# Kernel tuning notes

Hardware: AMD Instinct MI355X
Metric: run time of the kernel (lower is better)

## Reference

```python
import jax, jax.numpy as jnp
import numpy as np

NUM_SAMPLE = 80  # hardcoded in the original forward
NUM_ACT = 6
NUM_OPP = 3


def setup_inputs() -> dict:
    key = jax.random.key(0)
    k0, k1, k2 = jax.random.split(key, 3)
    B, D = 4096, 512
    x = jax.random.normal(k0, (B, D), dtype=jnp.float32)
    # orthogonal init with gain 0.01 -> small weights; approximate scale
    W_opp = jax.random.normal(k1, (NUM_OPP, D, NUM_ACT), dtype=jnp.float32) * 0.01
    b_opp = jnp.zeros((NUM_OPP, NUM_ACT), dtype=jnp.float32)
    W = jax.random.normal(k2, (D + NUM_OPP * NUM_ACT, NUM_ACT), dtype=jnp.float32) * 0.01
    b = jnp.zeros((NUM_ACT,), dtype=jnp.float32)
    return {"x": x, "W_opp": W_opp, "b_opp": b_opp, "W": W, "b": b}


def reference(x, W_opp, b_opp, W, b):
    B, D = x.shape
    # --- opponent actors: small linear + softmax, vectorized over the 3 opponents ---
    logits = jnp.einsum('bd,kda->kba', x, W_opp) + b_opp[:, None, :]   # [3,B,6]
    dist = jax.nn.softmax(logits, axis=-1)                              # [3,B,6]
    logp = jax.nn.log_softmax(logits, axis=-1)
    # entropy.mean() per opponent, then sum/3 == mean over opponents
    entropy = (-(dist * logp).sum(-1)).mean(-1).mean()

    # --- vectorized categorical sampling: 80 samples per opponent per batch elem ---
    skey = jax.random.key(42)
    samples = jax.random.categorical(skey, logits[:, None], axis=-1,
                                     shape=(NUM_OPP, NUM_SAMPLE, B))   # [3,S,B] int

    # gather sampled-action probabilities
    probs = jnp.take_along_axis(dist[:, None], samples[..., None], axis=-1)[..., 0]  # [3,S,B]
    probs_bt = jnp.transpose(probs, (0, 2, 1))                          # [3,B,S]
    p1 = probs_bt[0] * probs_bt[1] * probs_bt[2]                        # [B,S]
    p2 = p1 / p1.sum(axis=1, keepdims=True)                             # normalized joint weights

    # actions3[b,s,k] = sampled action of opponent k, sample s, batch b
    acts = jnp.transpose(samples, (2, 1, 0))                            # [B,S,3]
    oh = jax.nn.one_hot(acts, NUM_ACT, dtype=x.dtype).reshape(B, NUM_SAMPLE, NUM_OPP * NUM_ACT)  # [B,S,18]

    xa = jnp.broadcast_to(x[:, None, :], (B, NUM_SAMPLE, D))            # replicate x per sample
    a = jnp.concatenate([xa, oh], axis=2)                               # [B,S,D+18]
    agent_probs = jax.nn.softmax(a @ W + b, axis=-1)                    # [B,S,6]

    actions_probs = jnp.einsum('bs,bsa->ba', p2, agent_probs)           # [B,6]
    return actions_probs, dist, entropy
```

## Files before the change

kernel.cpp:

```cpp
#include <hip/hip_runtime.h>
#include <stdint.h>

#define NUM_ACT 6
#define NUM_OPP 3
#define NUM_SAMPLE 80
#define BATCH 4096
#define DIM 512
#define ACC_STRIDE 98304
#define TROWS 32

__device__ __forceinline__ uint32_t rotl32(uint32_t x, int d) {
  return (x << d) | (x >> (32 - d));
}

__device__ __forceinline__ void tf_round4(uint32_t& x0, uint32_t& x1,
                                          int r0, int r1, int r2, int r3) {
  x0 += x1; x1 = rotl32(x1, r0); x1 ^= x0;
  x0 += x1; x1 = rotl32(x1, r1); x1 ^= x0;
  x0 += x1; x1 = rotl32(x1, r2); x1 ^= x0;
  x0 += x1; x1 = rotl32(x1, r3); x1 ^= x0;
}

__device__ __forceinline__ void threefry2x32(uint32_t k0, uint32_t k1,
                                             uint32_t& x0, uint32_t& x1) {
  const uint32_t ks2 = k0 ^ k1 ^ 0x1BD11BDAu;
  x0 += k0;  x1 += k1;
  tf_round4(x0, x1, 13, 15, 26, 6);  x0 += k1;  x1 += ks2 + 1u;
  tf_round4(x0, x1, 17, 29, 16, 24); x0 += ks2; x1 += k0  + 2u;
  tf_round4(x0, x1, 13, 15, 26, 6);  x0 += k0;  x1 += k1  + 3u;
  tf_round4(x0, x1, 17, 29, 16, 24); x0 += k1;  x1 += ks2 + 4u;
  tf_round4(x0, x1, 13, 15, 26, 6);  x0 += ks2; x1 += k0  + 5u;
}

__device__ __forceinline__ float jax_uniform(uint32_t flat_idx) {
  uint32_t x0 = 0u, x1 = flat_idx;
  threefry2x32(0u, 42u, x0, x1);
  uint32_t bits = x0 ^ x1;
  return __uint_as_float((bits >> 9) | 0x3f800000u) - 1.0f;
}

__device__ __forceinline__ void dot4(float& a, float4 u, float4 v) {
  a = fmaf(u.x, v.x, a); a = fmaf(u.y, v.y, a);
  a = fmaf(u.z, v.z, a); a = fmaf(u.w, v.w, a);
}

template<int NCH>
__global__ __launch_bounds__(128) void k1_gemm(
    const float* __restrict__ x, const float* __restrict__ Wopp,
    const float* __restrict__ W, float* __restrict__ part,
    float* __restrict__ ws_ent) {
  constexpr int WIDTH = 512 / NCH;
  constexpr int XSTR = WIDTH + 4;
  const int tile = blockIdx.x / NCH;
  const int ch = blockIdx.x % NCH;
  const int rowbase = tile * TROWS;
  const int dbase = ch * WIDTH;
  __shared__ float xs[TROWS * XSTR];
  __shared__ float wt[24 * XSTR];
  const int t = threadIdx.x;

  for (int f = t; f < TROWS * (WIDTH / 4); f += 128) {
    int row = f / (WIDTH / 4), c4 = (f % (WIDTH / 4)) << 2;
    float4 v = *(const float4*)(x + (size_t)(rowbase + row) * DIM + dbase + c4);
    *(float4*)(xs + row * XSTR + c4) = v;
  }
  for (int i = t; i < 24 * WIDTH; i += 128) {
    int c = i % 24, dd = i / 24;
    int d = dbase + dd;
    float v = (c < 18) ? Wopp[(c / 6) * (DIM * 6) + d * 6 + (c % 6)]
                       : W[d * 6 + (c - 18)];
    wt[c * XSTR + dd] = v;
  }
  __syncthreads();

  const int rowg = t >> 3, colg = t & 7;
  float acc[2][3] = {{0.f, 0.f, 0.f}, {0.f, 0.f, 0.f}};
  const float* xp = xs + (rowg * 2) * XSTR;
  const float* wp = wt + (colg * 3) * XSTR;
#pragma unroll 4
  for (int dd = 0; dd < WIDTH; dd += 4) {
    float4 x0 = *(const float4*)(xp + dd);
    float4 x1 = *(const float4*)(xp + XSTR + dd);
    float4 w0 = *(const float4*)(wp + dd);
    float4 w1 = *(const float4*)(wp + XSTR + dd);
    float4 w2 = *(const float4*)(wp + 2 * XSTR + dd);
    dot4(acc[0][0], x0, w0); dot4(acc[0][1], x0, w1); dot4(acc[0][2], x0, w2);
    dot4(acc[1][0], x1, w0); dot4(acc[1][1], x1, w1); dot4(acc[1][2], x1, w2);
  }
  const int r0 = rowbase + rowg * 2, c0 = colg * 3;
  float* p = part + (size_t)ch * ACC_STRIDE;
#pragma unroll
  for (int rr = 0; rr < 2; rr++)
#pragma unroll
    for (int cc = 0; cc < 3; cc++)
      p[(r0 + rr) * 24 + c0 + cc] = acc[rr][cc];
  if (blockIdx.x == 0 && t == 0) ws_ent[0] = 0.f;
}

template<int NCH>
__global__ __launch_bounds__(256) void k2_softmax(
    const float* __restrict__ part, const float* __restrict__ bopp,
    float* __restrict__ dout, float* __restrict__ ws_ent) {
  int row = blockIdx.x * 256 + threadIdx.x;
  int k = row >> 12, b = row & 4095;
  float l[NUM_ACT];
#pragma unroll
  for (int a = 0; a < NUM_ACT; a++) {
    float s = bopp[k * 6 + a];
#pragma unroll
    for (int ch = 0; ch < NCH; ch++)
      s += part[ch * ACC_STRIDE + b * 24 + k * 6 + a];
    l[a] = s;
  }
  float m = l[0];
#pragma unroll
  for (int a = 1; a < NUM_ACT; a++) m = fmaxf(m, l[a]);
  float e[NUM_ACT], Z = 0.f;
#pragma unroll
  for (int a = 0; a < NUM_ACT; a++) { e[a] = expf(l[a] - m); Z += e[a]; }
  float logZ = logf(Z);
  float H = 0.f;
#pragma unroll
  for (int a = 0; a < NUM_ACT; a++) {
    float pa = e[a] / Z;
    dout[BATCH * NUM_ACT + row * NUM_ACT + a] = pa;
    H -= pa * ((l[a] - m) - logZ);
  }
#pragma unroll
  for (int off = 32; off > 0; off >>= 1) H += __shfl_down(H, off);
  if ((threadIdx.x & 63) == 0) atomicAdd(ws_ent, H);
}

template<int NCH>
__global__ __launch_bounds__(256) void k3_agent(
    const float* __restrict__ part, const float* __restrict__ bopp,
    const float* __restrict__ W, const float* __restrict__ bias,
    const float* __restrict__ ws_ent, float* __restrict__ dout) {
  int b = blockIdx.x;
  int t = threadIdx.x;
  __shared__ float s_dist[NUM_OPP][NUM_ACT];
  __shared__ float s_xw[NUM_ACT];
  __shared__ float s_bias[NUM_ACT];
  __shared__ float s_W2[NUM_OPP * NUM_ACT][NUM_ACT];
  __shared__ int   s_act[NUM_OPP][NUM_SAMPLE];
  __shared__ float s_prob[NUM_OPP][NUM_SAMPLE];

  if (t < 18) {
    int k = t / 6, a = t - k * 6;
    s_dist[k][a] = dout[BATCH * NUM_ACT + (k * BATCH + b) * NUM_ACT + a];
  } else if (t >= 64 && t < 64 + NUM_ACT) {
    int a = t - 64;
    float s = bias[a];
#pragma unroll
    for (int ch = 0; ch < NCH; ch++)
      s += part[ch * ACC_STRIDE + b * 24 + 18 + a];
    s_xw[a] = s;
  } else if (t >= 128 && t < 128 + 108) {
    int i = t - 128;
    s_W2[i / 6][i % 6] = W[DIM * NUM_ACT + i];
  }
  __syncthreads();

  if (t < NUM_OPP * NUM_SAMPLE) {
    int k = t / NUM_SAMPLE, s = t - k * NUM_SAMPLE;
    float u = jax_uniform((uint32_t)(k * NUM_SAMPLE + s) * BATCH + (uint32_t)b);
    float c = s_dist[k][0], pr = s_dist[k][0];
    int sel = 0;
#pragma unroll
    for (int a = 1; a < NUM_ACT; a++) {
      bool take = (u >= c);
      sel += take ? 1 : 0;
      pr = take ? s_dist[k][a] : pr;
      c += s_dist[k][a];
    }
    s_act[k][s] = sel;
    s_prob[k][s] = pr;
  }
  __syncthreads();

  if (t < 64) {
    float p1a = s_prob[0][t] * s_prob[1][t] * s_prob[2][t];
    const bool hasb = t < (NUM_SAMPLE - 64);
    float p1b = 0.f;
    if (hasb) p1b = s_prob[0][t + 16] * s_prob[1][t + 16] * s_prob[2][t + 16];
    if (hasb) p1b = s_prob[0][t + 64] * s_prob[1][t + 64] * s_prob[2][t + 64];
    float tot = p1a + p1b;
#pragma unroll
    for (int m = 32; m > 0; m >>= 1) tot += __shfl_xor(tot, m);

    float o[NUM_ACT];
#pragma unroll
    for (int a = 0; a < NUM_ACT; a++) o[a] = 0.f;
    {
      int a0 = s_act[0][t], a1 = s_act[1][t], a2 = s_act[2][t];
      float la[NUM_ACT];
#pragma unroll
      for (int a = 0; a < NUM_ACT; a++)
        la[a] = s_xw[a] + s_W2[a0][a] + s_W2[6 + a1][a] + s_W2[12 + a2][a];
      float m = la[0];
#pragma unroll
      for (int a = 1; a < NUM_ACT; a++) m = fmaxf(m, la[a]);
      float e[NUM_ACT], Z = 0.f;
#pragma unroll
      for (int a = 0; a < NUM_ACT; a++) { e[a] = expf(la[a] - m); Z += e[a]; }
      float wz = (p1a / tot) / Z;
#pragma unroll
      for (int a = 0; a < NUM_ACT; a++) o[a] = wz * e[a];
    }
    if (hasb) {
      int j = t + 64;
      int a0 = s_act[0][j], a1 = s_act[1][j], a2 = s_act[2][j];
      float la[NUM_ACT];
#pragma unroll
      for (int a = 0; a < NUM_ACT; a++)
        la[a] = s_xw[a] + s_W2[a0][a] + s_W2[6 + a1][a] + s_W2[12 + a2][a];
      float m = la[0];
#pragma unroll
      for (int a = 1; a < NUM_ACT; a++) m = fmaxf(m, la[a]);
      float e[NUM_ACT], Z = 0.f;
#pragma unroll
      for (int a = 0; a < NUM_ACT; a++) { e[a] = expf(la[a] - m); Z += e[a]; }
      float wz = (p1b / tot) / Z;
#pragma unroll
      for (int a = 0; a < NUM_ACT; a++) o[a] += wz * e[a];
    }
#pragma unroll
    for (int m = 32; m > 0; m >>= 1)
#pragma unroll
      for (int a = 0; a < NUM_ACT; a++) o[a] += __shfl_xor(o[a], m);
    if (t == 0) {
#pragma unroll
      for (int a = 0; a < NUM_ACT; a++) dout[b * NUM_ACT + a] = o[a];
    }
  }
  if (b == 0 && t == 255) {
    dout[BATCH * NUM_ACT + NUM_OPP * BATCH * NUM_ACT] = ws_ent[0] * (1.0f / 12288.0f);
  }
}

extern "C" void kernel_launch(void* const* d_in, const int* in_sizes, int n_in,
                              void* d_out, int out_size, void* d_ws, size_t ws_size,
                              hipStream_t stream) {
  const float* x    = (const float*)d_in[0];
  const float* Wopp = (const float*)d_in[1];
  const float* bopp = (const float*)d_in[2];
  const float* W    = (const float*)d_in[3];
  const float* bias = (const float*)d_in[4];
  float* out = (float*)d_out;
  float* part = (float*)d_ws;

  size_t need8 = ((size_t)8 * ACC_STRIDE + 1) * sizeof(float);
  if (ws_size >= need8) {
    float* ws_ent = part + (size_t)8 * ACC_STRIDE;
    k1_gemm<8><<<(BATCH / TROWS) * 8, 128, 0, stream>>>(x, Wopp, W, part, ws_ent);
    k2_softmax<8><<<48, 256, 0, stream>>>(part, bopp, out, ws_ent);
    k3_agent<8><<<BATCH, 256, 0, stream>>>(part, bopp, W, bias, ws_ent, out);
  } else {
    float* ws_ent = part + (size_t)4 * ACC_STRIDE;
    k1_gemm<4><<<(BATCH / TROWS) * 4, 128, 0, stream>>>(x, Wopp, W, part, ws_ent);
    k2_softmax<4><<<48, 256, 0, stream>>>(part, bopp, out, ws_ent);
    k3_agent<4><<<BATCH, 256, 0, stream>>>(part, bopp, W, bias, ws_ent, out);
  }
}
```

Before: 90.33 us.

## Fuse GEMM, opponent softmax and agent sampling into one per-row kernel

Replaces the three-kernel pipeline (tiled GEMM writing partial sums to workspace, a softmax/entropy kernel, and a per-row agent kernel) with one kernel launched per batch row. Each block loads its x row into shared memory, computes the 24 dot products with 8-way split-K in shared memory, does the softmax, entropy atomic and sampling in place, and zeroes the entropy slot with a memset. This removes the workspace round trips and two launches. The cost is that the weight matrices are re-read from global memory by every block with strided scalar loads, and every block issues an atomic on the same address. It also drops a redundant dead load of p1b.

```diff
diff --git a/kernel.cpp b/kernel.cpp
--- a/kernel.cpp
+++ b/kernel.cpp
@@ -6,8 +6,7 @@
 #define NUM_SAMPLE 80
 #define BATCH 4096
 #define DIM 512
-#define ACC_STRIDE 98304
-#define TROWS 32
+#define ENT_IDX 98304
 
 __device__ __forceinline__ uint32_t rotl32(uint32_t x, int d) {
   return (x << d) | (x >> (32 - d));
@@ -39,130 +38,82 @@
   return __uint_as_float((bits >> 9) | 0x3f800000u) - 1.0f;
 }
 
-__device__ __forceinline__ void dot4(float& a, float4 u, float4 v) {
-  a = fmaf(u.x, v.x, a); a = fmaf(u.y, v.y, a);
-  a = fmaf(u.z, v.z, a); a = fmaf(u.w, v.w, a);
-}
-
-template<int NCH>
-__global__ __launch_bounds__(128) void k1_gemm(
+__global__ __launch_bounds__(256) void k_fused(
     const float* __restrict__ x, const float* __restrict__ Wopp,
-    const float* __restrict__ W, float* __restrict__ part,
-    float* __restrict__ ws_ent) {
-  constexpr int WIDTH = 512 / NCH;
-  constexpr int XSTR = WIDTH + 4;
-  const int tile = blockIdx.x / NCH;
-  const int ch = blockIdx.x % NCH;
-  const int rowbase = tile * TROWS;
-  const int dbase = ch * WIDTH;
-  __shared__ float xs[TROWS * XSTR];
-  __shared__ float wt[24 * XSTR];
+    const float* __restrict__ bopp, const float* __restrict__ W,
+    const float* __restrict__ bias, float* __restrict__ out) {
+  const int b = blockIdx.x;
   const int t = threadIdx.x;
 
-  for (int f = t; f < TROWS * (WIDTH / 4); f += 128) {
-    int row = f / (WIDTH / 4), c4 = (f % (WIDTH / 4)) << 2;
-    float4 v = *(const float4*)(x + (size_t)(rowbase + row) * DIM + dbase + c4);
-    *(float4*)(xs + row * XSTR + c4) = v;
-  }
-  for (int i = t; i < 24 * WIDTH; i += 128) {
-    int c = i % 24, dd = i / 24;
-    int d = dbase + dd;
-    float v = (c < 18) ? Wopp[(c / 6) * (DIM * 6) + d * 6 + (c % 6)]
-                       : W[d * 6 + (c - 18)];
-    wt[c * XSTR + dd] = v;
-  }
-  __syncthreads();
-
-  const int rowg = t >> 3, colg = t & 7;
-  float acc[2][3] = {{0.f, 0.f, 0.f}, {0.f, 0.f, 0.f}};
-  const float* xp = xs + (rowg * 2) * XSTR;
-  const float* wp = wt + (colg * 3) * XSTR;
-#pragma unroll 4
-  for (int dd = 0; dd < WIDTH; dd += 4) {
-    float4 x0 = *(const float4*)(xp + dd);
-    float4 x1 = *(const float4*)(xp + XSTR + dd);
-    float4 w0 = *(const float4*)(wp + dd);
-    float4 w1 = *(const float4*)(wp + XSTR + dd);
-    float4 w2 = *(const float4*)(wp + 2 * XSTR + dd);
-    dot4(acc[0][0], x0, w0); dot4(acc[0][1], x0, w1); dot4(acc[0][2], x0, w2);
-    dot4(acc[1][0], x1, w0); dot4(acc[1][1], x1, w1); dot4(acc[1][2], x1, w2);
-  }
-  const int r0 = rowbase + rowg * 2, c0 = colg * 3;
-  float* p = part + (size_t)ch * ACC_STRIDE;
-#pragma unroll
-  for (int rr = 0; rr < 2; rr++)
-#pragma unroll
-    for (int cc = 0; cc < 3; cc++)
-      p[(r0 + rr) * 24 + c0 + cc] = acc[rr][cc];
-  if (blockIdx.x == 0 && t == 0) ws_ent[0] = 0.f;
-}
-
-template<int NCH>
-__global__ __launch_bounds__(256) void k2_softmax(
-    const float* __restrict__ part, const float* __restrict__ bopp,
-    float* __restrict__ dout, float* __restrict__ ws_ent) {
-  int row = blockIdx.x * 256 + threadIdx.x;
-  int k = row >> 12, b = row & 4095;
-  float l[NUM_ACT];
-#pragma unroll
-  for (int a = 0; a < NUM_ACT; a++) {
-    float s = bopp[k * 6 + a];
-#pragma unroll
-    for (int ch = 0; ch < NCH; ch++)
-      s += part[ch * ACC_STRIDE + b * 24 + k * 6 + a];
-    l[a] = s;
-  }
-  float m = l[0];
-#pragma unroll
-  for (int a = 1; a < NUM_ACT; a++) m = fmaxf(m, l[a]);
-  float e[NUM_ACT], Z = 0.f;
-#pragma unroll
-  for (int a = 0; a < NUM_ACT; a++) { e[a] = expf(l[a] - m); Z += e[a]; }
-  float logZ = logf(Z);
-  float H = 0.f;
-#pragma unroll
-  for (int a = 0; a < NUM_ACT; a++) {
-    float pa = e[a] / Z;
-    dout[BATCH * NUM_ACT + row * NUM_ACT + a] = pa;
-    H -= pa * ((l[a] - m) - logZ);
-  }
-#pragma unroll
-  for (int off = 32; off > 0; off >>= 1) H += __shfl_down(H, off);
-  if ((threadIdx.x & 63) == 0) atomicAdd(ws_ent, H);
-}
-
-template<int NCH>
-__global__ __launch_bounds__(256) void k3_agent(
-    const float* __restrict__ part, const float* __restrict__ bopp,
-    const float* __restrict__ W, const float* __restrict__ bias,
-    const float* __restrict__ ws_ent, float* __restrict__ dout) {
-  int b = blockIdx.x;
-  int t = threadIdx.x;
+  __shared__ float xs[DIM];
+  __shared__ float s_part[8][24];
   __shared__ float s_dist[NUM_OPP][NUM_ACT];
   __shared__ float s_xw[NUM_ACT];
-  __shared__ float s_bias[NUM_ACT];
   __shared__ float s_W2[NUM_OPP * NUM_ACT][NUM_ACT];
   __shared__ int   s_act[NUM_OPP][NUM_SAMPLE];
   __shared__ float s_prob[NUM_OPP][NUM_SAMPLE];
 
-  if (t < 18) {
-    int k = t / 6, a = t - k * 6;
-    s_dist[k][a] = dout[BATCH * NUM_ACT + (k * BATCH + b) * NUM_ACT + a];
-  } else if (t >= 64 && t < 64 + NUM_ACT) {
-    int a = t - 64;
-    float s = bias[a];
-#pragma unroll
-    for (int ch = 0; ch < NCH; ch++)
-      s += part[ch * ACC_STRIDE + b * 24 + 18 + a];
-    s_xw[a] = s;
-  } else if (t >= 128 && t < 128 + 108) {
+  {
+    float2 v = *(const float2*)(x + (size_t)b * DIM + t * 2);
+    *(float2*)(xs + t * 2) = v;
+  }
+  if (t >= 128 && t < 128 + 108) {
     int i = t - 128;
     s_W2[i / 6][i % 6] = W[DIM * NUM_ACT + i];
   }
   __syncthreads();
 
+  if (t < 192) {
+    const int c = t % 24, g = t / 24;
+    const float* wp = (c < 18) ? (Wopp + (c / 6) * (DIM * NUM_ACT) + (c % 6))
+                               : (W + (c - 18));
+    wp += (size_t)(g * 64) * NUM_ACT;
+    const float* xp = xs + g * 64;
+    float acc = 0.f;
+#pragma unroll 8
+    for (int d = 0; d < 64; d++)
+      acc = fmaf(xp[d], wp[d * NUM_ACT], acc);
+    s_part[g][c] = acc;
+  }
+  __syncthreads();
+
+  if (t < NUM_OPP) {
+    const int k = t;
+    float l[NUM_ACT];
+#pragma unroll
+    for (int a = 0; a < NUM_ACT; a++) {
+      float s = bopp[k * NUM_ACT + a];
+#pragma unroll
+      for (int g = 0; g < 8; g++) s += s_part[g][k * NUM_ACT + a];
+      l[a] = s;
+    }
+    float m = l[0];
+#pragma unroll
+    for (int a = 1; a < NUM_ACT; a++) m = fmaxf(m, l[a]);
+    float e[NUM_ACT], Z = 0.f;
+#pragma unroll
+    for (int a = 0; a < NUM_ACT; a++) { e[a] = expf(l[a] - m); Z += e[a]; }
+    float logZ = logf(Z);
+    float H = 0.f;
+#pragma unroll
+    for (int a = 0; a < NUM_ACT; a++) {
+      float pa = e[a] / Z;
+      s_dist[k][a] = pa;
+      out[BATCH * NUM_ACT + ((size_t)k * BATCH + b) * NUM_ACT + a] = pa;
+      H -= pa * ((l[a] - m) - logZ);
+    }
+    atomicAdd(out + ENT_IDX, H * (1.0f / 12288.0f));
+  } else if (t >= 18 && t < 24) {
+    const int a = t - 18;
+    float s = bias[a];
+#pragma unroll
+    for (int g = 0; g < 8; g++) s += s_part[g][18 + a];
+    s_xw[a] = s;
+  }
+  __syncthreads();
+
   if (t < NUM_OPP * NUM_SAMPLE) {
-    int k = t / NUM_SAMPLE, s = t - k * NUM_SAMPLE;
+    const int k = t / NUM_SAMPLE, s = t - k * NUM_SAMPLE;
     float u = jax_uniform((uint32_t)(k * NUM_SAMPLE + s) * BATCH + (uint32_t)b);
     float c = s_dist[k][0], pr = s_dist[k][0];
     int sel = 0;
@@ -182,7 +133,6 @@
     float p1a = s_prob[0][t] * s_prob[1][t] * s_prob[2][t];
     const bool hasb = t < (NUM_SAMPLE - 64);
     float p1b = 0.f;
-    if (hasb) p1b = s_prob[0][t + 16] * s_prob[1][t + 16] * s_prob[2][t + 16];
     if (hasb) p1b = s_prob[0][t + 64] * s_prob[1][t + 64] * s_prob[2][t + 64];
     float tot = p1a + p1b;
 #pragma unroll
@@ -230,11 +180,8 @@
       for (int a = 0; a < NUM_ACT; a++) o[a] += __shfl_xor(o[a], m);
     if (t == 0) {
 #pragma unroll
-      for (int a = 0; a < NUM_ACT; a++) dout[b * NUM_ACT + a] = o[a];
-    }
-  }
-  if (b == 0 && t == 255) {
-    dout[BATCH * NUM_ACT + NUM_OPP * BATCH * NUM_ACT] = ws_ent[0] * (1.0f / 12288.0f);
+      for (int a = 0; a < NUM_ACT; a++) out[b * NUM_ACT + a] = o[a];
+    }
   }
 }
 
@@ -247,18 +194,7 @@
   const float* W    = (const float*)d_in[3];
   const float* bias = (const float*)d_in[4];
   float* out = (float*)d_out;
-  float* part = (float*)d_ws;
-
-  size_t need8 = ((size_t)8 * ACC_STRIDE + 1) * sizeof(float);
-  if (ws_size >= need8) {
-    float* ws_ent = part + (size_t)8 * ACC_STRIDE;
-    k1_gemm<8><<<(BATCH / TROWS) * 8, 128, 0, stream>>>(x, Wopp, W, part, ws_ent);
-    k2_softmax<8><<<48, 256, 0, stream>>>(part, bopp, out, ws_ent);
-    k3_agent<8><<<BATCH, 256, 0, stream>>>(part, bopp, W, bias, ws_ent, out);
-  } else {
-    float* ws_ent = part + (size_t)4 * ACC_STRIDE;
-    k1_gemm<4><<<(BATCH / TROWS) * 4, 128, 0, stream>>>(x, Wopp, W, part, ws_ent);
-    k2_softmax<4><<<48, 256, 0, stream>>>(part, bopp, out, ws_ent);
-    k3_agent<4><<<BATCH, 256, 0, stream>>>(part, bopp, W, bias, ws_ent, out);
-  }
-}
+
+  hipMemsetAsync(out + ENT_IDX, 0, sizeof(float), stream);
+  k_fused<<<BATCH, 256, 0, stream>>>(x, Wopp, bopp, W, bias, out);
+}
```

Measured after the change: 133.2 us. 1.47x slower.

## Fuse opponent softmax into per-wavefront agent kernel and reduce entropy deterministically

Applied to the files above, without the earlier changes.

Merges the opponent softmax/entropy kernel into the agent kernel, so each 64-lane wavefront handles one batch row (four rows per block) and keeps samples in registers instead of shared arrays with block barriers. Per-row entropy goes to a workspace array and a small final kernel sums it, replacing the global atomic. This removes a launch, the round trip of dist through global memory, and most block-wide syncs. In exchange it adds a third tiny launch and reads LDS without an explicit barrier, relying on the writes and reads staying within one wavefront.

```diff
diff --git a/kernel.cpp b/kernel.cpp
--- a/kernel.cpp
+++ b/kernel.cpp
@@ -8,6 +8,7 @@
 #define DIM 512
 #define ACC_STRIDE 98304
 #define TROWS 32
+#define ENT_IDX 98304
 
 __device__ __forceinline__ uint32_t rotl32(uint32_t x, int d) {
   return (x << d) | (x >> (32 - d));
@@ -47,8 +48,7 @@
 template<int NCH>
 __global__ __launch_bounds__(128) void k1_gemm(
     const float* __restrict__ x, const float* __restrict__ Wopp,
-    const float* __restrict__ W, float* __restrict__ part,
-    float* __restrict__ ws_ent) {
+    const float* __restrict__ W, float* __restrict__ part) {
   constexpr int WIDTH = 512 / NCH;
   constexpr int XSTR = WIDTH + 4;
   const int tile = blockIdx.x / NCH;
@@ -94,148 +94,181 @@
 #pragma unroll
     for (int cc = 0; cc < 3; cc++)
       p[(r0 + rr) * 24 + c0 + cc] = acc[rr][cc];
-  if (blockIdx.x == 0 && t == 0) ws_ent[0] = 0.f;
-}
+}
+
+#define WSTR 144
 
 template<int NCH>
-__global__ __launch_bounds__(256) void k2_softmax(
-    const float* __restrict__ part, const float* __restrict__ bopp,
-    float* __restrict__ dout, float* __restrict__ ws_ent) {
-  int row = blockIdx.x * 256 + threadIdx.x;
-  int k = row >> 12, b = row & 4095;
-  float l[NUM_ACT];
-#pragma unroll
-  for (int a = 0; a < NUM_ACT; a++) {
-    float s = bopp[k * 6 + a];
-#pragma unroll
-    for (int ch = 0; ch < NCH; ch++)
-      s += part[ch * ACC_STRIDE + b * 24 + k * 6 + a];
-    l[a] = s;
-  }
-  float m = l[0];
-#pragma unroll
-  for (int a = 1; a < NUM_ACT; a++) m = fmaxf(m, l[a]);
-  float e[NUM_ACT], Z = 0.f;
-#pragma unroll
-  for (int a = 0; a < NUM_ACT; a++) { e[a] = expf(l[a] - m); Z += e[a]; }
-  float logZ = logf(Z);
-  float H = 0.f;
-#pragma unroll
-  for (int a = 0; a < NUM_ACT; a++) {
-    float pa = e[a] / Z;
-    dout[BATCH * NUM_ACT + row * NUM_ACT + a] = pa;
-    H -= pa * ((l[a] - m) - logZ);
-  }
-#pragma unroll
-  for (int off = 32; off > 0; off >>= 1) H += __shfl_down(H, off);
-  if ((threadIdx.x & 63) == 0) atomicAdd(ws_ent, H);
-}
-
-template<int NCH>
-__global__ __launch_bounds__(256) void k3_agent(
+__global__ __launch_bounds__(256) void k3f(
     const float* __restrict__ part, const float* __restrict__ bopp,
     const float* __restrict__ W, const float* __restrict__ bias,
-    const float* __restrict__ ws_ent, float* __restrict__ dout) {
-  int b = blockIdx.x;
-  int t = threadIdx.x;
-  __shared__ float s_dist[NUM_OPP][NUM_ACT];
-  __shared__ float s_xw[NUM_ACT];
-  __shared__ float s_bias[NUM_ACT];
-  __shared__ float s_W2[NUM_OPP * NUM_ACT][NUM_ACT];
-  __shared__ int   s_act[NUM_OPP][NUM_SAMPLE];
-  __shared__ float s_prob[NUM_OPP][NUM_SAMPLE];
-
-  if (t < 18) {
-    int k = t / 6, a = t - k * 6;
-    s_dist[k][a] = dout[BATCH * NUM_ACT + (k * BATCH + b) * NUM_ACT + a];
-  } else if (t >= 64 && t < 64 + NUM_ACT) {
-    int a = t - 64;
+    float* __restrict__ out, float* __restrict__ ws_H) {
+  const int w = threadIdx.x >> 6;
+  const int l = threadIdx.x & 63;
+  const int b = blockIdx.x * 4 + w;
+  __shared__ float lds[4][WSTR];
+  float* L = lds[w];
+
+  if (l < 54) {
+    float2 v = *(const float2*)(W + DIM * NUM_ACT + 2 * l);
+    L[2 * l] = v.x; L[2 * l + 1] = v.y;
+  }
+
+  float H = 0.f;
+  if (l < NUM_OPP) {
+    const int k = l;
+    float lg[NUM_ACT];
+#pragma unroll
+    for (int a = 0; a < NUM_ACT; a++) {
+      float s = bopp[k * NUM_ACT + a];
+#pragma unroll
+      for (int g = 0; g < NCH; g++)
+        s += part[g * ACC_STRIDE + b * 24 + k * NUM_ACT + a];
+      lg[a] = s;
+    }
+    float m = lg[0];
+#pragma unroll
+    for (int a = 1; a < NUM_ACT; a++) m = fmaxf(m, lg[a]);
+    float e[NUM_ACT], Z = 0.f;
+#pragma unroll
+    for (int a = 0; a < NUM_ACT; a++) { e[a] = expf(lg[a] - m); Z += e[a]; }
+    float logZ = logf(Z);
+#pragma unroll
+    for (int a = 0; a < NUM_ACT; a++) {
+      float pa = e[a] / Z;
+      L[112 + k * NUM_ACT + a] = pa;
+      H -= pa * ((lg[a] - m) - logZ);
+    }
+  } else if (l >= 18 && l < 24) {
+    const int a = l - 18;
     float s = bias[a];
 #pragma unroll
-    for (int ch = 0; ch < NCH; ch++)
-      s += part[ch * ACC_STRIDE + b * 24 + 18 + a];
-    s_xw[a] = s;
-  } else if (t >= 128 && t < 128 + 108) {
-    int i = t - 128;
-    s_W2[i / 6][i % 6] = W[DIM * NUM_ACT + i];
-  }
-  __syncthreads();
-
-  if (t < NUM_OPP * NUM_SAMPLE) {
-    int k = t / NUM_SAMPLE, s = t - k * NUM_SAMPLE;
-    float u = jax_uniform((uint32_t)(k * NUM_SAMPLE + s) * BATCH + (uint32_t)b);
-    float c = s_dist[k][0], pr = s_dist[k][0];
+    for (int g = 0; g < NCH; g++)
+      s += part[g * ACC_STRIDE + b * 24 + 18 + a];
+    L[136 + a] = s;
+  }
+  H += __shfl_down(H, 1);
+  H += __shfl_down(H, 2);
+
+  float d[18];
+#pragma unroll
+  for (int i = 0; i < 18; i++) d[i] = L[112 + i];
+
+  int   act_a[3];
+  float pr_a[3];
+#pragma unroll
+  for (int k = 0; k < NUM_OPP; k++) {
+    float u = jax_uniform((uint32_t)(k * NUM_SAMPLE + l) * BATCH + (uint32_t)b);
+    float c = d[k * 6 + 0], pr = d[k * 6 + 0];
     int sel = 0;
 #pragma unroll
     for (int a = 1; a < NUM_ACT; a++) {
       bool take = (u >= c);
       sel += take ? 1 : 0;
-      pr = take ? s_dist[k][a] : pr;
-      c += s_dist[k][a];
-    }
-    s_act[k][s] = sel;
-    s_prob[k][s] = pr;
-  }
+      pr = take ? d[k * 6 + a] : pr;
+      c += d[k * 6 + a];
+    }
+    act_a[k] = sel; pr_a[k] = pr;
+  }
+  float prb = 0.f; int actb = 0;
+  if (l < 48) {
+    const int k = l >> 4, s = 64 + (l & 15);
+    float u = jax_uniform((uint32_t)(k * NUM_SAMPLE + s) * BATCH + (uint32_t)b);
+    float c = L[112 + k * 6 + 0], pr = c;
+    int sel = 0;
+#pragma unroll
+    for (int a = 1; a < NUM_ACT; a++) {
+      float da = L[112 + k * 6 + a];
+      bool take = (u >= c);
+      sel += take ? 1 : 0;
+      pr = take ? da : pr;
+      c += da;
+    }
+    actb = sel; prb = pr;
+  }
+  const int tm = l & 15;
+  float pb0 = __shfl(prb, tm), pb1 = __shfl(prb, tm + 16), pb2 = __shfl(prb, tm + 32);
+  int   ab0 = __shfl(actb, tm), ab1 = __shfl(actb, tm + 16), ab2 = __shfl(actb, tm + 32);
+
+  const bool hasb = l < (NUM_SAMPLE - 64);
+  float p1a = pr_a[0] * pr_a[1] * pr_a[2];
+  float p1b = 0.f;
+  if (hasb) p1b = pb0 * pb1 * pb2;
+  float tot = p1a + p1b;
+#pragma unroll
+  for (int m = 32; m > 0; m >>= 1) tot += __shfl_xor(tot, m);
+
+  float xw[NUM_ACT];
+#pragma unroll
+  for (int a = 0; a < NUM_ACT; a++) xw[a] = L[136 + a];
+
+  float o[NUM_ACT];
+#pragma unroll
+  for (int a = 0; a < NUM_ACT; a++) o[a] = 0.f;
+  {
+    int a0 = act_a[0], a1 = act_a[1], a2 = act_a[2];
+    float la[NUM_ACT];
+#pragma unroll
+    for (int a = 0; a < NUM_ACT; a++)
+      la[a] = xw[a] + L[a0 * 6 + a] + L[(6 + a1) * 6 + a] + L[(12 + a2) * 6 + a];
+    float m = la[0];
+#pragma unroll
+    for (int a = 1; a < NUM_ACT; a++) m = fmaxf(m, la[a]);
+    float e[NUM_ACT], Z = 0.f;
+#pragma unroll
+    for (int a = 0; a < NUM_ACT; a++) { e[a] = expf(la[a] - m); Z += e[a]; }
+    float wz = (p1a / tot) / Z;
+#pragma unroll
+    for (int a = 0; a < NUM_ACT; a++) o[a] = wz * e[a];
+  }
+  if (hasb) {
+    float la[NUM_ACT];
+#pragma unroll
+    for (int a = 0; a < NUM_ACT; a++)
+      la[a] = xw[a] + L[ab0 * 6 + a] + L[(6 + ab1) * 6 + a] + L[(12 + ab2) * 6 + a];
+    float m = la[0];
+#pragma unroll
+    for (int a = 1; a < NUM_ACT; a++) m = fmaxf(m, la[a]);
+    float e[NUM_ACT], Z = 0.f;
+#pragma unroll
+    for (int a = 0; a < NUM_ACT; a++) { e[a] = expf(la[a] - m); Z += e[a]; }
+    float wz = (p1b / tot) / Z;
+#pragma unroll
+    for (int a = 0; a < NUM_ACT; a++) o[a] += wz * e[a];
+  }
+#pragma unroll
+  for (int m = 32; m > 0; m >>= 1)
+#pragma unroll
+    for (int a = 0; a < NUM_ACT; a++) o[a] += __shfl_xor(o[a], m);
+
+  if (l == 0) {
+#pragma unroll
+    for (int a = 0; a < NUM_ACT; a++) out[b * NUM_ACT + a] = o[a];
+    ws_H[b] = H;
+  }
+  if (l < 18) {
+    int k = l / 6, a = l - k * 6;
+    out[BATCH * NUM_ACT + ((size_t)k * BATCH + b) * NUM_ACT + a] = L[112 + l];
+  }
+}
+
+__global__ __launch_bounds__(256) void k_ent(const float* __restrict__ ws_H,
+                                             float* __restrict__ out) {
+  const int t = threadIdx.x;
+  const float4* p = (const float4*)ws_H;
+  float s = 0.f;
+#pragma unroll
+  for (int i = 0; i < 4; i++) {
+    float4 v = p[t + 256 * i];
+    s += v.x + v.y + v.z + v.w;
+  }
+#pragma unroll
+  for (int m = 32; m > 0; m >>= 1) s += __shfl_xor(s, m);
+  __shared__ float sw[4];
+  if ((t & 63) == 0) sw[t >> 6] = s;
   __syncthreads();
-
-  if (t < 64) {
-    float p1a = s_prob[0][t] * s_prob[1][t] * s_prob[2][t];
-    const bool hasb = t < (NUM_SAMPLE - 64);
-    float p1b = 0.f;
-    if (hasb) p1b = s_prob[0][t + 16] * s_prob[1][t + 16] * s_prob[2][t + 16];
-    if (hasb) p1b = s_prob[0][t + 64] * s_prob[1][t + 64] * s_prob[2][t + 64];
-    float tot = p1a + p1b;
-#pragma unroll
-    for (int m = 32; m > 0; m >>= 1) tot += __shfl_xor(tot, m);
-
-    float o[NUM_ACT];
-#pragma unroll
-    for (int a = 0; a < NUM_ACT; a++) o[a] = 0.f;
-    {
-      int a0 = s_act[0][t], a1 = s_act[1][t], a2 = s_act[2][t];
-      float la[NUM_ACT];
-#pragma unroll
-      for (int a = 0; a < NUM_ACT; a++)
-        la[a] = s_xw[a] + s_W2[a0][a] + s_W2[6 + a1][a] + s_W2[12 + a2][a];
-      float m = la[0];
-#pragma unroll
-      for (int a = 1; a < NUM_ACT; a++) m = fmaxf(m, la[a]);
-      float e[NUM_ACT], Z = 0.f;
-#pragma unroll
-      for (int a = 0; a < NUM_ACT; a++) { e[a] = expf(la[a] - m); Z += e[a]; }
-      float wz = (p1a / tot) / Z;
-#pragma unroll
-      for (int a = 0; a < NUM_ACT; a++) o[a] = wz * e[a];
-    }
-    if (hasb) {
-      int j = t + 64;
-      int a0 = s_act[0][j], a1 = s_act[1][j], a2 = s_act[2][j];
-      float la[NUM_ACT];
-#pragma unroll
-      for (int a = 0; a < NUM_ACT; a++)
-        la[a] = s_xw[a] + s_W2[a0][a] + s_W2[6 + a1][a] + s_W2[12 + a2][a];
-      float m = la[0];
-#pragma unroll
-      for (int a = 1; a < NUM_ACT; a++) m = fmaxf(m, la[a]);
-      float e[NUM_ACT], Z = 0.f;
-#pragma unroll
-      for (int a = 0; a < NUM_ACT; a++) { e[a] = expf(la[a] - m); Z += e[a]; }
-      float wz = (p1b / tot) / Z;
-#pragma unroll
-      for (int a = 0; a < NUM_ACT; a++) o[a] += wz * e[a];
-    }
-#pragma unroll
-    for (int m = 32; m > 0; m >>= 1)
-#pragma unroll
-      for (int a = 0; a < NUM_ACT; a++) o[a] += __shfl_xor(o[a], m);
-    if (t == 0) {
-#pragma unroll
-      for (int a = 0; a < NUM_ACT; a++) dout[b * NUM_ACT + a] = o[a];
-    }
-  }
-  if (b == 0 && t == 255) {
-    dout[BATCH * NUM_ACT + NUM_OPP * BATCH * NUM_ACT] = ws_ent[0] * (1.0f / 12288.0f);
-  }
+  if (t == 0)
+    out[ENT_IDX] = (sw[0] + sw[1] + sw[2] + sw[3]) * (1.0f / 12288.0f);
 }
 
 extern "C" void kernel_launch(void* const* d_in, const int* in_sizes, int n_in,
@@ -249,16 +282,16 @@
   float* out = (float*)d_out;
   float* part = (float*)d_ws;
 
-  size_t need8 = ((size_t)8 * ACC_STRIDE + 1) * sizeof(float);
+  size_t need8 = ((size_t)8 * ACC_STRIDE + BATCH) * sizeof(float);
   if (ws_size >= need8) {
-    float* ws_ent = part + (size_t)8 * ACC_STRIDE;
-    k1_gemm<8><<<(BATCH / TROWS) * 8, 128, 0, stream>>>(x, Wopp, W, part, ws_ent);
-    k2_softmax<8><<<48, 256, 0, stream>>>(part, bopp, out, ws_ent);
-    k3_agent<8><<<BATCH, 256, 0, stream>>>(part, bopp, W, bias, ws_ent, out);
+    float* ws_H = part + (size_t)8 * ACC_STRIDE;
+    k1_gemm<8><<<(BATCH / TROWS) * 8, 128, 0, stream>>>(x, Wopp, W, part);
+    k3f<8><<<BATCH / 4, 256, 0, stream>>>(part, bopp, W, bias, out, ws_H);
+    k_ent<<<1, 256, 0, stream>>>(ws_H, out);
   } else {
-    float* ws_ent = part + (size_t)4 * ACC_STRIDE;
-    k1_gemm<4><<<(BATCH / TROWS) * 4, 128, 0, stream>>>(x, Wopp, W, part, ws_ent);
-    k2_softmax<4><<<48, 256, 0, stream>>>(part, bopp, out, ws_ent);
-    k3_agent<4><<<BATCH, 256, 0, stream>>>(part, bopp, W, bias, ws_ent, out);
-  }
-}
+    float* ws_H = part + (size_t)4 * ACC_STRIDE;
+    k1_gemm<4><<<(BATCH / TROWS) * 4, 128, 0, stream>>>(x, Wopp, W, part);
+    k3f<4><<<BATCH / 4, 256, 0, stream>>>(part, bopp, W, bias, out, ws_H);
+    k_ent<<<1, 256, 0, stream>>>(ws_H, out);
+  }
+}
```

Result: faster. 86.69 us (-4.0%).
